# Kernel optimization log

Hardware: AMD Instinct MI355X
Metric: run time of the kernel (lower is better)

The kernel has to match this reference:

```python
import jax, jax.numpy as jnp
import numpy as np

N_NODES = 50000
M_ITEMS = 5000
D_FEAT = 64      # graph node feature dim (input_size)
D_HID = 32       # input_size // 2
D_EMB = 64       # embedding_size = output_size
N_EDGES = 1200000
BATCH = 4096


def _sage_conv(h, src, dst, W_l, b_l, W_r, n_nodes):
    # PyG SAGEConv (mean aggr, root_weight=True):
    # out_i = W_l @ mean_{j in N(i)} h_j + b_l + W_r @ h_i
    msg = h[src]                                              # [E, Din]
    agg = jax.ops.segment_sum(msg, dst, num_segments=n_nodes)  # [N, Din]
    deg = jax.ops.segment_sum(jnp.ones((src.shape[0],), h.dtype), dst,
                              num_segments=n_nodes)
    agg = agg / jnp.maximum(deg, 1.0)[:, None]
    return agg @ W_l.T + b_l + h @ W_r.T


def setup_inputs() -> dict:
    key = jax.random.key(0)
    ks = jax.random.split(key, 12)
    x = jax.random.randint(ks[0], (BATCH,), 0, N_NODES)
    node_x = jax.random.normal(ks[1], (N_NODES, D_FEAT), dtype=jnp.float32)
    edge_index = jax.random.randint(ks[2], (2, N_EDGES), 0, N_NODES)
    rating_mat = jax.random.uniform(ks[3], (N_NODES, M_ITEMS), dtype=jnp.float32)
    s = 0.05
    W_enc = jax.random.normal(ks[4], (D_EMB, M_ITEMS), dtype=jnp.float32) * s
    b_enc = jnp.zeros((D_EMB,), jnp.float32)
    W_dec = jax.random.normal(ks[5], (M_ITEMS, D_EMB), dtype=jnp.float32) * s
    b_dec = jnp.zeros((M_ITEMS,), jnp.float32)
    Wl1 = jax.random.normal(ks[6], (D_HID, D_FEAT), dtype=jnp.float32) * s
    bl1 = jnp.zeros((D_HID,), jnp.float32)
    Wr1 = jax.random.normal(ks[7], (D_HID, D_FEAT), dtype=jnp.float32) * s
    Wl2 = jax.random.normal(ks[8], (D_EMB, D_HID), dtype=jnp.float32) * s
    bl2 = jnp.zeros((D_EMB,), jnp.float32)
    Wr2 = jax.random.normal(ks[9], (D_EMB, D_HID), dtype=jnp.float32) * s
    return {"x": x, "node_x": node_x, "edge_index": edge_index,
            "rating_mat": rating_mat, "W_enc": W_enc, "b_enc": b_enc,
            "W_dec": W_dec, "b_dec": b_dec, "Wl1": Wl1, "bl1": bl1,
            "Wr1": Wr1, "Wl2": Wl2, "bl2": bl2, "Wr2": Wr2}


def reference(x, node_x, edge_index, rating_mat, W_enc, b_enc, W_dec, b_dec,
              Wl1, bl1, Wr1, Wl2, bl2, Wr2):
    src, dst = edge_index[0], edge_index[1]
    # Graph branch (training path, dropout omitted for determinism)
    h = _sage_conv(node_x, src, dst, Wl1, bl1, Wr1, N_NODES)   # [N, D_HID]
    h = jax.nn.relu(h)
    emb_all = _sage_conv(h, src, dst, Wl2, bl2, Wr2, N_NODES)  # [N, D_EMB]
    emb_graph = emb_all[x]                                      # [B, D_EMB]
    # Autoencoder branch
    items = rating_mat[x]                                       # [B, M]
    emb_ae = items @ W_enc.T + b_enc                            # [B, D_EMB]
    out = jax.nn.sigmoid(emb_graph + emb_ae)                    # method='add'
    out = jax.nn.sigmoid(out @ W_dec.T + b_dec)                 # [B, M]
    return out
```

## Files before the change

kernel.cpp:

```cpp
#include <hip/hip_runtime.h>
#include <math.h>

#define N_NODES 50000
#define M_ITEMS 5000
#define D_FEAT 64
#define D_HID 32
#define D_EMB 64
#define N_EDGES 1200000
#define BATCH 4096
#define CAP 80
#define KCH 10
#define KW  500

__device__ __forceinline__ float sigmoidf_(float z) {
    return 1.0f / (1.0f + __expf(-z));
}

#define FILL_BLOCKS  ((N_EDGES + 255) / 256)
#define XW_BLOCKS    ((N_NODES * D_HID + 255) / 256)
#define TR_BLOCKS    ((D_EMB * M_ITEMS + 255) / 256)

__global__ __launch_bounds__(256)
void k_mega1(const int* __restrict__ src, const int* __restrict__ dst,
             int* __restrict__ cursor, int* __restrict__ slot,
             const float* __restrict__ Wenc, float* __restrict__ WencT,
             const float* __restrict__ node_x, const float* __restrict__ Wl1,
             float* __restrict__ y1) {
    __shared__ float wsT[D_FEAT * D_HID];
    const int bid = blockIdx.x;
    if (bid < FILL_BLOCKS) {
        int e = bid * 256 + threadIdx.x;
        if (e < N_EDGES) {
            int dn = dst[e];
            int pos = atomicAdd(&cursor[dn], 1);
            if (pos < CAP) slot[(size_t)dn * CAP + pos] = src[e];
        }
        return;
    }
    if (bid < FILL_BLOCKS + XW_BLOCKS) {
        for (int j = threadIdx.x; j < D_FEAT * D_HID; j += 256) {
            int c = j >> 6, k = j & 63;
            wsT[k * D_HID + c] = Wl1[j];
        }
        __syncthreads();
        int idx = (bid - FILL_BLOCKS) * 256 + threadIdx.x;
        if (idx >= N_NODES * D_HID) return;
        int r = idx >> 5, c = idx & 31;
        const float* xp = node_x + (size_t)r * D_FEAT;
        float s = 0.f;
#pragma unroll
        for (int k = 0; k < D_FEAT; k += 4) {
            float4 xv = *reinterpret_cast<const float4*>(xp + k);
            s = fmaf(xv.x, wsT[(k + 0) * D_HID + c], s);
            s = fmaf(xv.y, wsT[(k + 1) * D_HID + c], s);
            s = fmaf(xv.z, wsT[(k + 2) * D_HID + c], s);
            s = fmaf(xv.w, wsT[(k + 3) * D_HID + c], s);
        }
        y1[idx] = s;
        return;
    }
    {
        int idx = (bid - FILL_BLOCKS - XW_BLOCKS) * 256 + threadIdx.x;
        if (idx >= D_EMB * M_ITEMS) return;
        int e = idx & 63, m = idx >> 6;
        WencT[idx] = Wenc[(size_t)e * M_ITEMS + m];
    }
}

__device__ __forceinline__ int pick4_32(int s0, int s1, int s2, int s3, int j) {
    int v = (j < 32) ? s0 : (j < 64) ? s1 : (j < 96) ? s2 : s3;
    return __shfl(v, j & 31, 32);
}

__global__ __launch_bounds__(256)
void k_node1(const float* __restrict__ node_x, const float* __restrict__ y1,
             const int* __restrict__ cursor, const int* __restrict__ slot,
             const float* __restrict__ Wr1, const float* __restrict__ bl1,
             float* __restrict__ h) {
    __shared__ float wt[D_FEAT * D_HID];
    for (int j = threadIdx.x; j < D_HID * D_FEAT; j += 256) {
        int c = j >> 6, k = j & 63;
        wt[k * D_HID + c] = Wr1[j];
    }
    __syncthreads();
    const int lane = threadIdx.x & 31;
    const int n = blockIdx.x * 8 + (threadIdx.x >> 5);
    const int dgf = cursor[n];
    const int dg = min(dgf, CAP);
    const int* sl = slot + (size_t)n * CAP;
    int s0 = (lane < dg) ? sl[lane] : 0;
    int s1 = (32 + lane < dg) ? sl[32 + lane] : 0;
    int s2 = (64 + lane < dg) ? sl[64 + lane] : 0;
    int s3 = 0;
    float g0 = 0.f, g1 = 0.f, g2 = 0.f, g3 = 0.f;
    int j = 0;
    for (; j + 4 <= dg; j += 4) {
        int a = pick4_32(s0, s1, s2, s3, j);
        int b = pick4_32(s0, s1, s2, s3, j + 1);
        int c = pick4_32(s0, s1, s2, s3, j + 2);
        int d = pick4_32(s0, s1, s2, s3, j + 3);
        g0 += y1[(size_t)a * D_HID + lane];
        g1 += y1[(size_t)b * D_HID + lane];
        g2 += y1[(size_t)c * D_HID + lane];
        g3 += y1[(size_t)d * D_HID + lane];
    }
    for (; j < dg; ++j)
        g0 += y1[(size_t)pick4_32(s0, s1, s2, s3, j) * D_HID + lane];
    float g = ((g0 + g1) + (g2 + g3)) / fmaxf((float)dgf, 1.f) + bl1[lane];
    const float* xp = node_x + (size_t)n * D_FEAT;
    float s = 0.f;
#pragma unroll
    for (int k = 0; k < D_FEAT; k += 4) {
        float4 xv = *reinterpret_cast<const float4*>(xp + k);
        s = fmaf(xv.x, wt[(k + 0) * D_HID + lane], s);
        s = fmaf(xv.y, wt[(k + 1) * D_HID + lane], s);
        s = fmaf(xv.z, wt[(k + 2) * D_HID + lane], s);
        s = fmaf(xv.w, wt[(k + 3) * D_HID + lane], s);
    }
    h[(size_t)n * D_HID + lane] = fmaxf(g + s, 0.f);
}

__global__ __launch_bounds__(512)
void k_enc_part(const int* __restrict__ x, const float* __restrict__ rating,
                const float* __restrict__ WencT, float* __restrict__ part) {
    __shared__ float sm[8192];
    __shared__ int ns[16];
    const int tid = threadIdx.x, lane = tid & 63, wv = tid >> 6;
    const int rb = blockIdx.x * 16;
    const int ky = blockIdx.y;
    if (tid < 16) ns[tid] = x[rb + tid];
    __syncthreads();
    int nh[16];
#pragma unroll
    for (int i = 0; i < 16; ++i)
        nh[i] = __builtin_amdgcn_readfirstlane(ns[i]);
    for (int j4 = tid; j4 < 2000; j4 += 512) {
        int row = j4 / 125, c4 = j4 - row * 125;
        float4 v = *reinterpret_cast<const float4*>(
            rating + (size_t)nh[row] * M_ITEMS + ky * KW + c4 * 4);
        *reinterpret_cast<float4*>(&sm[row * KW + c4 * 4]) = v;
    }
    __syncthreads();
    float acc[16];
#pragma unroll
    for (int i = 0; i < 16; ++i) acc[i] = 0.f;
    for (int g = wv; g < 125; g += 8) {
        int ml = g * 4, gm = ky * KW + ml;
        float w0 = WencT[(size_t)(gm + 0) * 64 + lane];
        float w1 = WencT[(size_t)(gm + 1) * 64 + lane];
        float w2 = WencT[(size_t)(gm + 2) * 64 + lane];
        float w3 = WencT[(size_t)(gm + 3) * 64 + lane];
#pragma unroll
        for (int r = 0; r < 16; ++r) {
            float4 rv = *reinterpret_cast<const float4*>(&sm[r * KW + ml]);
            acc[r] = fmaf(rv.x, w0, acc[r]);
            acc[r] = fmaf(rv.y, w1, acc[r]);
            acc[r] = fmaf(rv.z, w2, acc[r]);
            acc[r] = fmaf(rv.w, w3, acc[r]);
        }
    }
    __syncthreads();
#pragma unroll
    for (int r = 0; r < 16; ++r) sm[(wv * 16 + r) * 64 + lane] = acc[r];
    __syncthreads();
#pragma unroll
    for (int half = 0; half < 2; ++half) {
        int r = wv * 2 + half;
        float s = 0.f;
#pragma unroll
        for (int w = 0; w < 8; ++w) s += sm[(w * 16 + r) * 64 + lane];
        part[((size_t)ky * BATCH + rb + r) * 64 + lane] = s;
    }
}

__global__ __launch_bounds__(512)
void k_comb(const int* __restrict__ x, const float* __restrict__ part,
            const float* __restrict__ benc, const int* __restrict__ cursor,
            const int* __restrict__ slot, const float* __restrict__ h,
            const float* __restrict__ Wl2, const float* __restrict__ bl2,
            const float* __restrict__ Wr2, float* __restrict__ emb) {
    __shared__ float wl2t[D_HID * D_EMB];
    __shared__ float wr2t[D_HID * D_EMB];
    __shared__ float aggl[8][D_HID];
    __shared__ float hl[8][D_HID];
    __shared__ int ns[8];
    const int tid = threadIdx.x, lane = tid & 63, wv = tid >> 6;
    const int rb = blockIdx.x * 8;
    if (tid < 8) ns[tid] = x[rb + tid];
    for (int j = tid; j < D_EMB * D_HID; j += 512) {
        int e = j >> 5, k = j & 31;
        wl2t[k * D_EMB + e] = Wl2[j];
        wr2t[k * D_EMB + e] = Wr2[j];
    }
    __syncthreads();
    const int row = rb + wv;
    const int node = __builtin_amdgcn_readfirstlane(ns[wv]);
    float ae = benc[lane];
#pragma unroll
    for (int ky = 0; ky < KCH; ++ky)
        ae += part[((size_t)ky * BATCH + row) * 64 + lane];
    const int k32 = lane & 31, hi = lane >> 5;
    const int dgf = cursor[node];
    const int dg = min(dgf, CAP);
    const int* sl = slot + (size_t)node * CAP;
    float a0 = 0.f, a1 = 0.f, a2 = 0.f, a3 = 0.f;
    int t = 0;
    for (; t + 8 <= dg; t += 8) {
        int e0 = sl[t + 0], e1 = sl[t + 1], e2 = sl[t + 2], e3 = sl[t + 3];
        int e4 = sl[t + 4], e5 = sl[t + 5], e6 = sl[t + 6], e7 = sl[t + 7];
        int n0 = hi ? e1 : e0;
        int n1 = hi ? e3 : e2;
        int n2 = hi ? e5 : e4;
        int n3 = hi ? e7 : e6;
        a0 += h[(size_t)n0 * D_HID + k32];
        a1 += h[(size_t)n1 * D_HID + k32];
        a2 += h[(size_t)n2 * D_HID + k32];
        a3 += h[(size_t)n3 * D_HID + k32];
    }
    for (; t < dg; t += 2) {
        int e0 = sl[t];
        int e1 = (t + 1 < dg) ? sl[t + 1] : e0;
        int nb = hi ? e1 : e0;
        if (t + hi < dg) a0 += h[(size_t)nb * D_HID + k32];
    }
    float g = (a0 + a1) + (a2 + a3);
    g += __shfl(g, lane ^ 32, 64);
    if (lane < 32) {
        aggl[wv][k32] = g / fmaxf((float)dgf, 1.f);
        hl[wv][k32] = h[(size_t)node * D_HID + k32];
    }
    float ge = bl2[lane];
#pragma unroll
    for (int k = 0; k < D_HID; ++k)
        ge = fmaf(aggl[wv][k], wl2t[k * D_EMB + lane], ge);
#pragma unroll
    for (int k = 0; k < D_HID; ++k)
        ge = fmaf(hl[wv][k], wr2t[k * D_EMB + lane], ge);
    emb[(size_t)row * D_EMB + lane] = sigmoidf_(ge + ae);
}

__global__ __launch_bounds__(256)
void k_dec(const float* __restrict__ emb, const float* __restrict__ Wdec,
           const float* __restrict__ bdec, float* __restrict__ out) {
    const int tid = threadIdx.x;
    const int b0 = blockIdx.y * 32;
    const int m = blockIdx.x * 256 + tid;
    if (m >= M_ITEMS) return;
    const float* ep = emb + (size_t)b0 * 64;
    float acc[32];
#pragma unroll
    for (int i = 0; i < 32; ++i) acc[i] = 0.f;
    const float* wp = Wdec + (size_t)m * 64;
#pragma unroll
    for (int k = 0; k < 64; k += 4) {
        float4 w = *reinterpret_cast<const float4*>(&wp[k]);
#pragma unroll
        for (int i = 0; i < 32; ++i) {
            float4 e4 = *reinterpret_cast<const float4*>(ep + i * 64 + k);
            acc[i] = fmaf(w.x, e4.x, acc[i]);
            acc[i] = fmaf(w.y, e4.y, acc[i]);
            acc[i] = fmaf(w.z, e4.z, acc[i]);
            acc[i] = fmaf(w.w, e4.w, acc[i]);
        }
    }
    float bb = bdec[m];
#pragma unroll
    for (int i = 0; i < 32; ++i)
        out[(size_t)(b0 + i) * M_ITEMS + m] = sigmoidf_(acc[i] + bb);
}

extern "C" void kernel_launch(void* const* d_in, const int* in_sizes, int n_in,
                              void* d_out, int out_size, void* d_ws, size_t ws_size,
                              hipStream_t stream) {
    const int*   x      = (const int*)d_in[0];
    const float* node_x = (const float*)d_in[1];
    const int*   ei     = (const int*)d_in[2];
    const float* rating = (const float*)d_in[3];
    const float* Wenc   = (const float*)d_in[4];
    const float* benc   = (const float*)d_in[5];
    const float* Wdec   = (const float*)d_in[6];
    const float* bdec   = (const float*)d_in[7];
    const float* Wl1    = (const float*)d_in[8];
    const float* bl1    = (const float*)d_in[9];
    const float* Wr1    = (const float*)d_in[10];
    const float* Wl2    = (const float*)d_in[11];
    const float* bl2    = (const float*)d_in[12];
    const float* Wr2    = (const float*)d_in[13];
    const int* src = ei;
    const int* dst = ei + N_EDGES;

    char* w = (char*)d_ws;
    int*   cursor = (int*)w;   w += (size_t)N_NODES * 4;
    int*   slot   = (int*)w;   w += (size_t)N_NODES * CAP * 4;
    float* y1     = (float*)w; w += (size_t)N_NODES * D_HID * 4;
    float* h      = (float*)w; w += (size_t)N_NODES * D_HID * 4;
    float* emb    = (float*)w; w += (size_t)BATCH * D_EMB * 4;
    float* WencT  = (float*)w; w += (size_t)M_ITEMS * D_EMB * 4;
    float* part   = (float*)w; w += (size_t)KCH * BATCH * D_EMB * 4;

    hipMemsetAsync(cursor, 0, (size_t)N_NODES * 4, stream);

    k_mega1<<<FILL_BLOCKS + XW_BLOCKS + TR_BLOCKS, 256, 0, stream>>>(
        src, dst, cursor, slot, Wenc, WencT, node_x, Wl1, y1);
    k_node1<<<N_NODES / 8, 256, 0, stream>>>(
        node_x, y1, cursor, slot, Wr1, bl1, h);
    dim3 genc(BATCH / 16, KCH);
    k_enc_part<<<genc, 512, 0, stream>>>(x, rating, WencT, part);
    k_comb<<<BATCH / 8, 512, 0, stream>>>(
        x, part, benc, cursor, slot, h, Wl2, bl2, Wr2, emb);
    dim3 gdec((M_ITEMS + 255) / 256, BATCH / 32);
    k_dec<<<gdec, 256, 0, stream>>>(emb, Wdec, bdec, (float*)d_out);
}
```

Baseline: 296.5 us.

## Use bf16 MFMA for decoder GEMM with prepacked weights and restructure gathers

The fp32 FMA decoder is replaced with a bf16 MFMA 16x16x32 kernel. The decoder weights are converted once into an MFMA-ready bf16 layout inside the setup megakernel, and the combined embedding is written in bf16. The neighbor-gather kernels also change: node1 now processes two nodes per 64-lane wave and stages node features in shared memory, and comb uses a unified masked gather loop. These aim to cut decoder ALU cost and improve gather occupancy. The trade-off is bf16 rounding error and smaller, less coalesced output stores of 16 contiguous items per row.

```diff
diff --git a/kernel.cpp b/kernel.cpp
--- a/kernel.cpp
+++ b/kernel.cpp
@@ -11,21 +11,35 @@
 #define CAP 80
 #define KCH 10
 #define KW  500
+#define MCH 313
+
+typedef unsigned short u16;
+typedef unsigned int u32;
+typedef __attribute__((ext_vector_type(8))) short bf16x8;
+typedef __attribute__((ext_vector_type(4))) float f32x4;
 
 __device__ __forceinline__ float sigmoidf_(float z) {
     return 1.0f / (1.0f + __expf(-z));
+}
+__device__ __forceinline__ u16 f2bf(float f) {
+    u32 b = __float_as_uint(f);
+    b += 0x7FFFu + ((b >> 16) & 1u);
+    return (u16)(b >> 16);
 }
 
 #define FILL_BLOCKS  ((N_EDGES + 255) / 256)
 #define XW_BLOCKS    ((N_NODES * D_HID + 255) / 256)
 #define TR_BLOCKS    ((D_EMB * M_ITEMS + 255) / 256)
+#define WB_THREADS   (MCH * 2 * 64)
+#define WB_BLOCKS    ((WB_THREADS + 255) / 256)
 
 __global__ __launch_bounds__(256)
 void k_mega1(const int* __restrict__ src, const int* __restrict__ dst,
              int* __restrict__ cursor, int* __restrict__ slot,
              const float* __restrict__ Wenc, float* __restrict__ WencT,
              const float* __restrict__ node_x, const float* __restrict__ Wl1,
-             float* __restrict__ y1) {
+             float* __restrict__ y1, const float* __restrict__ Wdec,
+             uint4* __restrict__ WdecB) {
     __shared__ float wsT[D_FEAT * D_HID];
     const int bid = blockIdx.x;
     if (bid < FILL_BLOCKS) {
@@ -39,7 +53,7 @@
     }
     if (bid < FILL_BLOCKS + XW_BLOCKS) {
         for (int j = threadIdx.x; j < D_FEAT * D_HID; j += 256) {
-            int c = j >> 6, k = j & 63;
+            int c = j / D_FEAT, k = j % D_FEAT;
             wsT[k * D_HID + c] = Wl1[j];
         }
         __syncthreads();
@@ -59,17 +73,32 @@
         y1[idx] = s;
         return;
     }
-    {
+    if (bid < FILL_BLOCKS + XW_BLOCKS + TR_BLOCKS) {
         int idx = (bid - FILL_BLOCKS - XW_BLOCKS) * 256 + threadIdx.x;
         if (idx >= D_EMB * M_ITEMS) return;
         int e = idx & 63, m = idx >> 6;
         WencT[idx] = Wenc[(size_t)e * M_ITEMS + m];
-    }
-}
-
-__device__ __forceinline__ int pick4_32(int s0, int s1, int s2, int s3, int j) {
-    int v = (j < 32) ? s0 : (j < 64) ? s1 : (j < 96) ? s2 : s3;
-    return __shfl(v, j & 31, 32);
+        return;
+    }
+    {
+        int g = (bid - FILL_BLOCKS - XW_BLOCKS - TR_BLOCKS) * 256 + threadIdx.x;
+        if (g >= WB_THREADS) return;
+        int lane = g & 63, sq = g >> 6;
+        int step = sq & 1, chunk = sq >> 1;
+        int m = chunk * 16 + (lane & 15);
+        int k0 = step * 32 + ((lane >> 4) << 3);
+        u32 p0 = 0, p1 = 0, p2 = 0, p3 = 0;
+        if (m < M_ITEMS) {
+            const float* wp = Wdec + (size_t)m * 64 + k0;
+            float4 f0 = *reinterpret_cast<const float4*>(wp);
+            float4 f1 = *reinterpret_cast<const float4*>(wp + 4);
+            p0 = (u32)f2bf(f0.x) | ((u32)f2bf(f0.y) << 16);
+            p1 = (u32)f2bf(f0.z) | ((u32)f2bf(f0.w) << 16);
+            p2 = (u32)f2bf(f1.x) | ((u32)f2bf(f1.y) << 16);
+            p3 = (u32)f2bf(f1.z) | ((u32)f2bf(f1.w) << 16);
+        }
+        WdecB[g] = make_uint4(p0, p1, p2, p3);
+    }
 }
 
 __global__ __launch_bounds__(256)
@@ -78,46 +107,51 @@
              const float* __restrict__ Wr1, const float* __restrict__ bl1,
              float* __restrict__ h) {
     __shared__ float wt[D_FEAT * D_HID];
-    for (int j = threadIdx.x; j < D_HID * D_FEAT; j += 256) {
+    __shared__ float xsh[8][64];
+    const int tid = threadIdx.x;
+    for (int j = tid; j < D_HID * D_FEAT; j += 256) {
         int c = j >> 6, k = j & 63;
         wt[k * D_HID + c] = Wr1[j];
     }
-    __syncthreads();
-    const int lane = threadIdx.x & 31;
-    const int n = blockIdx.x * 8 + (threadIdx.x >> 5);
-    const int dgf = cursor[n];
-    const int dg = min(dgf, CAP);
-    const int* sl = slot + (size_t)n * CAP;
-    int s0 = (lane < dg) ? sl[lane] : 0;
-    int s1 = (32 + lane < dg) ? sl[32 + lane] : 0;
-    int s2 = (64 + lane < dg) ? sl[64 + lane] : 0;
-    int s3 = 0;
-    float g0 = 0.f, g1 = 0.f, g2 = 0.f, g3 = 0.f;
-    int j = 0;
-    for (; j + 4 <= dg; j += 4) {
-        int a = pick4_32(s0, s1, s2, s3, j);
-        int b = pick4_32(s0, s1, s2, s3, j + 1);
-        int c = pick4_32(s0, s1, s2, s3, j + 2);
-        int d = pick4_32(s0, s1, s2, s3, j + 3);
-        g0 += y1[(size_t)a * D_HID + lane];
-        g1 += y1[(size_t)b * D_HID + lane];
-        g2 += y1[(size_t)c * D_HID + lane];
-        g3 += y1[(size_t)d * D_HID + lane];
-    }
-    for (; j < dg; ++j)
-        g0 += y1[(size_t)pick4_32(s0, s1, s2, s3, j) * D_HID + lane];
-    float g = ((g0 + g1) + (g2 + g3)) / fmaxf((float)dgf, 1.f) + bl1[lane];
-    const float* xp = node_x + (size_t)n * D_FEAT;
-    float s = 0.f;
+    const int nb = blockIdx.x * 8;
+    for (int j = tid; j < 8 * 64; j += 256)
+        xsh[j >> 6][j & 63] = node_x[(size_t)(nb + (j >> 6)) * D_FEAT + (j & 63)];
+    __syncthreads();
+    const int lane = tid & 63, wv = tid >> 6;
+    const int k32 = lane & 31, hi = lane >> 5;
+    const int nA = nb + wv * 2, nB = nA + 1;
+    const int dgfA = cursor[nA], dgfB = cursor[nB];
+    const int dgA = min(dgfA, CAP), dgB = min(dgfB, CAP);
+    const int mx = max(dgA, dgB);
+    const int* slA = slot + (size_t)nA * CAP;
+    const int* slB = slot + (size_t)nB * CAP;
+    const int dgv = hi ? dgB : dgA;
+    float a0 = 0.f, a1 = 0.f, a2 = 0.f, a3 = 0.f;
+    for (int j = 0; j < mx; j += 4) {
+#pragma unroll
+        for (int i = 0; i < 4; ++i) {
+            int sA = (j + i < dgA) ? slA[j + i] : 0;
+            int sB = (j + i < dgB) ? slB[j + i] : 0;
+            int nbr = hi ? sB : sA;
+            float v = y1[(size_t)nbr * D_HID + k32];
+            float vm = (j + i < dgv) ? v : 0.f;
+            if (i == 0) a0 += vm; else if (i == 1) a1 += vm;
+            else if (i == 2) a2 += vm; else a3 += vm;
+        }
+    }
+    float g = (a0 + a1) + (a2 + a3);
+    const int my = wv * 2 + hi;
+    const float dgfv = (float)(hi ? dgfB : dgfA);
+    float s = g / fmaxf(dgfv, 1.f) + bl1[k32];
 #pragma unroll
     for (int k = 0; k < D_FEAT; k += 4) {
-        float4 xv = *reinterpret_cast<const float4*>(xp + k);
-        s = fmaf(xv.x, wt[(k + 0) * D_HID + lane], s);
-        s = fmaf(xv.y, wt[(k + 1) * D_HID + lane], s);
-        s = fmaf(xv.z, wt[(k + 2) * D_HID + lane], s);
-        s = fmaf(xv.w, wt[(k + 3) * D_HID + lane], s);
-    }
-    h[(size_t)n * D_HID + lane] = fmaxf(g + s, 0.f);
+        float4 xv = *reinterpret_cast<const float4*>(&xsh[my][k]);
+        s = fmaf(xv.x, wt[(k + 0) * D_HID + k32], s);
+        s = fmaf(xv.y, wt[(k + 1) * D_HID + k32], s);
+        s = fmaf(xv.z, wt[(k + 2) * D_HID + k32], s);
+        s = fmaf(xv.w, wt[(k + 3) * D_HID + k32], s);
+    }
+    h[(size_t)(nb + my) * D_HID + k32] = fmaxf(s, 0.f);
 }
 
 __global__ __launch_bounds__(512)
@@ -178,7 +212,7 @@
             const float* __restrict__ benc, const int* __restrict__ cursor,
             const int* __restrict__ slot, const float* __restrict__ h,
             const float* __restrict__ Wl2, const float* __restrict__ bl2,
-            const float* __restrict__ Wr2, float* __restrict__ emb) {
+            const float* __restrict__ Wr2, u16* __restrict__ emb_bf) {
     __shared__ float wl2t[D_HID * D_EMB];
     __shared__ float wr2t[D_HID * D_EMB];
     __shared__ float aggl[8][D_HID];
@@ -204,24 +238,18 @@
     const int dg = min(dgf, CAP);
     const int* sl = slot + (size_t)node * CAP;
     float a0 = 0.f, a1 = 0.f, a2 = 0.f, a3 = 0.f;
-    int t = 0;
-    for (; t + 8 <= dg; t += 8) {
-        int e0 = sl[t + 0], e1 = sl[t + 1], e2 = sl[t + 2], e3 = sl[t + 3];
-        int e4 = sl[t + 4], e5 = sl[t + 5], e6 = sl[t + 6], e7 = sl[t + 7];
-        int n0 = hi ? e1 : e0;
-        int n1 = hi ? e3 : e2;
-        int n2 = hi ? e5 : e4;
-        int n3 = hi ? e7 : e6;
-        a0 += h[(size_t)n0 * D_HID + k32];
-        a1 += h[(size_t)n1 * D_HID + k32];
-        a2 += h[(size_t)n2 * D_HID + k32];
-        a3 += h[(size_t)n3 * D_HID + k32];
-    }
-    for (; t < dg; t += 2) {
-        int e0 = sl[t];
-        int e1 = (t + 1 < dg) ? sl[t + 1] : e0;
-        int nb = hi ? e1 : e0;
-        if (t + hi < dg) a0 += h[(size_t)nb * D_HID + k32];
+    for (int t = 0; t < dg; t += 8) {
+#pragma unroll
+        for (int i = 0; i < 4; ++i) {
+            int j2 = t + 2 * i;
+            int sE = (j2 < dg) ? sl[j2] : 0;
+            int sO = (j2 + 1 < dg) ? sl[j2 + 1] : 0;
+            int nbr = hi ? sO : sE;
+            float v = h[(size_t)nbr * D_HID + k32];
+            float vm = (j2 + hi < dg) ? v : 0.f;
+            if (i == 0) a0 += vm; else if (i == 1) a1 += vm;
+            else if (i == 2) a2 += vm; else a3 += vm;
+        }
     }
     float g = (a0 + a1) + (a2 + a3);
     g += __shfl(g, lane ^ 32, 64);
@@ -236,37 +264,34 @@
 #pragma unroll
     for (int k = 0; k < D_HID; ++k)
         ge = fmaf(hl[wv][k], wr2t[k * D_EMB + lane], ge);
-    emb[(size_t)row * D_EMB + lane] = sigmoidf_(ge + ae);
+    emb_bf[(size_t)row * D_EMB + lane] = f2bf(sigmoidf_(ge + ae));
 }
 
 __global__ __launch_bounds__(256)
-void k_dec(const float* __restrict__ emb, const float* __restrict__ Wdec,
+void k_dec(const u16* __restrict__ emb_bf, const bf16x8* __restrict__ WdecB,
            const float* __restrict__ bdec, float* __restrict__ out) {
-    const int tid = threadIdx.x;
-    const int b0 = blockIdx.y * 32;
-    const int m = blockIdx.x * 256 + tid;
-    if (m >= M_ITEMS) return;
-    const float* ep = emb + (size_t)b0 * 64;
-    float acc[32];
-#pragma unroll
-    for (int i = 0; i < 32; ++i) acc[i] = 0.f;
-    const float* wp = Wdec + (size_t)m * 64;
-#pragma unroll
-    for (int k = 0; k < 64; k += 4) {
-        float4 w = *reinterpret_cast<const float4*>(&wp[k]);
-#pragma unroll
-        for (int i = 0; i < 32; ++i) {
-            float4 e4 = *reinterpret_cast<const float4*>(ep + i * 64 + k);
-            acc[i] = fmaf(w.x, e4.x, acc[i]);
-            acc[i] = fmaf(w.y, e4.y, acc[i]);
-            acc[i] = fmaf(w.z, e4.z, acc[i]);
-            acc[i] = fmaf(w.w, e4.w, acc[i]);
-        }
-    }
-    float bb = bdec[m];
-#pragma unroll
-    for (int i = 0; i < 32; ++i)
-        out[(size_t)(b0 + i) * M_ITEMS + m] = sigmoidf_(acc[i] + bb);
+    const int tid = threadIdx.x, lane = tid & 63, wv = tid >> 6;
+    const int q = blockIdx.x * 4 + wv;
+    if (q >= MCH) return;
+    const int r0 = blockIdx.y * 16;
+    const int row = r0 + (lane & 15);
+    const int kq = (lane >> 4) << 3;
+    const u16* ea = emb_bf + (size_t)row * 64 + kq;
+    bf16x8 A0 = *reinterpret_cast<const bf16x8*>(ea);
+    bf16x8 A1 = *reinterpret_cast<const bf16x8*>(ea + 32);
+    bf16x8 B0 = WdecB[(size_t)(q * 2 + 0) * 64 + lane];
+    bf16x8 B1 = WdecB[(size_t)(q * 2 + 1) * 64 + lane];
+    f32x4 c = {0.f, 0.f, 0.f, 0.f};
+    c = __builtin_amdgcn_mfma_f32_16x16x32_bf16(A0, B0, c, 0, 0, 0);
+    c = __builtin_amdgcn_mfma_f32_16x16x32_bf16(A1, B1, c, 0, 0, 0);
+    const int m = q * 16 + (lane & 15);
+    if (m < M_ITEMS) {
+        float bb = bdec[m];
+        const int rbase = r0 + (lane >> 4) * 4;
+#pragma unroll
+        for (int i = 0; i < 4; ++i)
+            out[(size_t)(rbase + i) * M_ITEMS + m] = sigmoidf_(c[i] + bb);
+    }
 }
 
 extern "C" void kernel_launch(void* const* d_in, const int* in_sizes, int n_in,
@@ -294,20 +319,22 @@
     int*   slot   = (int*)w;   w += (size_t)N_NODES * CAP * 4;
     float* y1     = (float*)w; w += (size_t)N_NODES * D_HID * 4;
     float* h      = (float*)w; w += (size_t)N_NODES * D_HID * 4;
-    float* emb    = (float*)w; w += (size_t)BATCH * D_EMB * 4;
+    u16*   emb_bf = (u16*)w;   w += (size_t)BATCH * D_EMB * 2;
     float* WencT  = (float*)w; w += (size_t)M_ITEMS * D_EMB * 4;
     float* part   = (float*)w; w += (size_t)KCH * BATCH * D_EMB * 4;
+    uint4* WdecB  = (uint4*)w; w += (size_t)WB_THREADS * 16;
 
     hipMemsetAsync(cursor, 0, (size_t)N_NODES * 4, stream);
 
-    k_mega1<<<FILL_BLOCKS + XW_BLOCKS + TR_BLOCKS, 256, 0, stream>>>(
-        src, dst, cursor, slot, Wenc, WencT, node_x, Wl1, y1);
+    k_mega1<<<FILL_BLOCKS + XW_BLOCKS + TR_BLOCKS + WB_BLOCKS, 256, 0, stream>>>(
+        src, dst, cursor, slot, Wenc, WencT, node_x, Wl1, y1, Wdec, WdecB);
     k_node1<<<N_NODES / 8, 256, 0, stream>>>(
         node_x, y1, cursor, slot, Wr1, bl1, h);
     dim3 genc(BATCH / 16, KCH);
     k_enc_part<<<genc, 512, 0, stream>>>(x, rating, WencT, part);
     k_comb<<<BATCH / 8, 512, 0, stream>>>(
-        x, part, benc, cursor, slot, h, Wl2, bl2, Wr2, emb);
-    dim3 gdec((M_ITEMS + 255) / 256, BATCH / 32);
-    k_dec<<<gdec, 256, 0, stream>>>(emb, Wdec, bdec, (float*)d_out);
-}
+        x, part, benc, cursor, slot, h, Wl2, bl2, Wr2, emb_bf);
+    dim3 gdec((MCH + 3) / 4, BATCH / 16);
+    k_dec<<<gdec, 256, 0, stream>>>(emb_bf, (const bf16x8*)WdecB, bdec,
+                                    (float*)d_out);
+}
```

Result: no change. 296.6 us (median of 3 runs) (+0.0%).
